# Performance work log

Hardware: AMD Instinct MI355X
Metric: run time of the kernel (lower is better)

Reference implementation:

```python
import jax, jax.numpy as jnp
import numpy as np

C_IN, C_OUT, KH, KW = 64, 128, 3, 3
STRIDE, PAD, DIL = 1, 1, 1
EPS = 1e-5


def setup_inputs() -> dict:
    key = jax.random.key(0)
    ks = jax.random.split(key, 7)
    B, H, W = 8, 112, 112
    x = jax.random.normal(ks[0], (B, C_IN, H, W), dtype=jnp.float32)
    # offset conv: produces 2*KH*KW offset channels; small init keeps offsets sane
    w_off = jax.random.normal(ks[1], (2 * KH * KW, C_IN, KH, KW), dtype=jnp.float32) * 0.01
    b_off = jax.random.normal(ks[2], (2 * KH * KW,), dtype=jnp.float32) * 0.01
    # deformable conv weight/bias
    fan_in = C_IN * KH * KW
    w_dcn = jax.random.normal(ks[3], (C_OUT, C_IN, KH, KW), dtype=jnp.float32) / np.sqrt(fan_in)
    b_dcn = jax.random.normal(ks[4], (C_OUT,), dtype=jnp.float32) * 0.01
    gamma = jnp.ones((C_OUT,), dtype=jnp.float32)
    beta = jnp.zeros((C_OUT,), dtype=jnp.float32)
    return {"x": x, "w_off": w_off, "b_off": b_off, "w_dcn": w_dcn,
            "b_dcn": b_dcn, "gamma": gamma, "beta": beta}


def _conv2d(x, w, b):
    y = jax.lax.conv_general_dilated(
        x, w, window_strides=(STRIDE, STRIDE),
        padding=((PAD, PAD), (PAD, PAD)),
        rhs_dilation=(DIL, DIL),
        dimension_numbers=("NCHW", "OIHW", "NCHW"))
    return y + b[None, :, None, None]


def _deform_conv(x, offset, w, b):
    # x: [B,C,H,W]; offset: [B, 2*KH*KW, Ho, Wo] with (dy, dx) pairs per tap
    B, C, H, W = x.shape
    KK = KH * KW
    Ho, Wo = offset.shape[2], offset.shape[3]
    off = offset.reshape(B, KK, 2, Ho, Wo)
    ky = (jnp.arange(KK) // KW).astype(jnp.float32)  # kernel row per tap
    kx = (jnp.arange(KK) % KW).astype(jnp.float32)
    base_y = (jnp.arange(Ho) * STRIDE - PAD).astype(jnp.float32)
    base_x = (jnp.arange(Wo) * STRIDE - PAD).astype(jnp.float32)
    # sampling positions [B, KK, Ho, Wo]
    py = off[:, :, 0] + base_y[None, None, :, None] + (ky * DIL)[None, :, None, None]
    px = off[:, :, 1] + base_x[None, None, None, :] + (kx * DIL)[None, :, None, None]

    y0 = jnp.floor(py)
    x0 = jnp.floor(px)
    wy1 = py - y0  # weight for y0+1
    wx1 = px - x0
    y0i = y0.astype(jnp.int32)
    x0i = x0.astype(jnp.int32)

    x_flat = x.reshape(B, C, H * W)

    def gather_corner(yi, xi, wgt):
        # yi, xi, wgt: [B, KK, Ho, Wo]
        valid = (yi >= 0) & (yi < H) & (xi >= 0) & (xi < W)
        idx = jnp.clip(yi, 0, H - 1) * W + jnp.clip(xi, 0, W - 1)
        idx = idx.reshape(B, -1)  # [B, KK*Ho*Wo]
        vals = jnp.take_along_axis(x_flat, idx[:, None, :], axis=2)  # [B, C, N]
        coef = (wgt * valid.astype(wgt.dtype)).reshape(B, 1, -1)
        return vals * coef

    samp = (gather_corner(y0i,     x0i,     (1 - wy1) * (1 - wx1))
            + gather_corner(y0i,     x0i + 1, (1 - wy1) * wx1)
            + gather_corner(y0i + 1, x0i,     wy1 * (1 - wx1))
            + gather_corner(y0i + 1, x0i + 1, wy1 * wx1))
    samp = samp.reshape(B, C, KK, Ho, Wo)
    out = jnp.einsum("bckhw,ock->bohw", samp, w.reshape(w.shape[0], C, KK))
    return out + b[None, :, None, None]


def reference(x, w_off, b_off, w_dcn, b_dcn, gamma, beta):
    offset = _conv2d(x, w_off, b_off)
    y = _deform_conv(x, offset, w_dcn, b_dcn)
    # BatchNorm2d (training mode: biased batch stats) + ReLU
    mean = jnp.mean(y, axis=(0, 2, 3))
    var = jnp.var(y, axis=(0, 2, 3))
    yhat = (y - mean[None, :, None, None]) * jax.lax.rsqrt(var + EPS)[None, :, None, None]
    y = gamma[None, :, None, None] * yhat + beta[None, :, None, None]
    return jax.nn.relu(y)
```

## Files before the change

kernel.cpp:

```cpp
#include <hip/hip_runtime.h>

#define H    112
#define W    112
#define HW   12544
#define CIN  64
#define COUT 128
#define BATCH 8
#define KK   9
#define OFFC 18
#define EPS  1e-5f
#define TP   32
#define KDIM 576
#define KHALF 288
#define KPAD2 296
#define NB   3136
#define YST  40
#define SSTRIDE 16

typedef unsigned short ushort;
typedef unsigned int uint;
typedef __attribute__((ext_vector_type(8))) short short8;
typedef __attribute__((ext_vector_type(4))) float floatx4;
typedef __attribute__((ext_vector_type(2))) float f32x2;

__device__ __forceinline__ ushort f2bf(float f) {
  uint u = __float_as_uint(f);
  u = (u + 0x7FFFu + ((u >> 16) & 1u)) >> 16;
  return (ushort)u;
}

__device__ __forceinline__ uint pack_bf2(float f0, float f1) {
  uint u0 = __float_as_uint(f0) + 0x8000u;
  uint u1 = __float_as_uint(f1) + 0x8000u;
  return __builtin_amdgcn_perm(u1, u0, 0x07060302u);
}

__device__ __forceinline__ f32x2 up2(uint u) {
  f32x2 r;
  r.x = __uint_as_float(u << 16);
  r.y = __uint_as_float(u & 0xFFFF0000u);
  return r;
}

__device__ __forceinline__ int tile196(int bx) {
  int xcd = bx & 7, q = bx >> 3;
  return (xcd < 4) ? xcd * 25 + q : 100 + (xcd - 4) * 24 + q;
}

__global__ __launch_bounds__(256) void k_prep(
    const float* __restrict__ x, const float* __restrict__ w_off,
    const float* __restrict__ w_dcn, ushort* __restrict__ xTb,
    ushort* __restrict__ w_offT, ushort* __restrict__ w_mf,
    float* __restrict__ stats) {
  if (blockIdx.y < BATCH) {
    __shared__ float tile[64][65];
    int b = blockIdx.y;
    int p0 = tile196(blockIdx.x) * 64;
    int tid = threadIdx.x;
    int j = tid & 63, cb = tid >> 6;
#pragma unroll
    for (int i = 0; i < 16; ++i) {
      int ci = cb * 16 + i;
      tile[ci][j] = x[((size_t)(b * CIN + ci)) * HW + p0 + j];
    }
    __syncthreads();
    int px = tid >> 2, ciq = tid & 3;
#pragma unroll
    for (int g = 0; g < 4; ++g) {
      int ci = ciq * 16 + g * 4;
      uint lo = pack_bf2(tile[ci + 0][px], tile[ci + 1][px]);
      uint hi = pack_bf2(tile[ci + 2][px], tile[ci + 3][px]);
      *(uint2*)&xTb[((size_t)b * HW + p0 + px) * 64 + ci] = make_uint2(lo, hi);
    }
  } else {
    int tid = threadIdx.x;
    if (blockIdx.x == 0) {
#pragma unroll
      for (int i = tid; i < 256 * SSTRIDE; i += 256) stats[i] = 0.f;
    }
    const int TOT = 32 * KDIM + COUT * KDIM;
    for (int i = blockIdx.x * 256 + tid; i < TOT; i += 196 * 256) {
      if (i < 32 * KDIM) {
        int oc = i / KDIM, k = i - oc * KDIM;
        int kk = k >> 6, ci = k & 63;
        float v = (oc < OFFC) ? w_off[(oc * CIN + ci) * KK + kk] : 0.f;
        w_offT[i] = f2bf(v);
      } else {
        int jj = i - 32 * KDIM;
        int co = jj / KDIM, k = jj - co * KDIM;
        int h2 = k / KHALF, r = k - h2 * KHALF;
        int kk = r >> 5, cil = r & 31;
        int ci = h2 * 32 + cil;
        w_mf[jj] = f2bf(w_dcn[(co * CIN + ci) * KK + kk]);
      }
    }
  }
}

__global__ __launch_bounds__(256) void k_offset_conv(
    const ushort* __restrict__ xTb, const ushort* __restrict__ w_offT,
    const float* __restrict__ bias, float* __restrict__ out) {
  int b = blockIdx.y;
  int wave = threadIdx.x >> 6, lane = threadIdx.x & 63;
  int row16 = lane & 15, quad = lane >> 4;
  int p = tile196(blockIdx.x) * 64 + wave * 16 + row16;
  int ho = p / W, wo = p - ho * W;
  const ushort* xb = xTb + (size_t)b * HW * 64;

  short8 Bf[18];
#pragma unroll
  for (int ks = 0; ks < 18; ++ks) {
    int kk = ks >> 1;
    int ci0 = (ks & 1) * 32 + quad * 8;
    int kh = kk / 3, kw = kk - kh * 3;
    int yy = ho + kh - 1, xx = wo + kw - 1;
    bool valid = (yy >= 0) & (yy < H) & (xx >= 0) & (xx < W);
    short8 v = {0, 0, 0, 0, 0, 0, 0, 0};
    if (valid) v = *(const short8*)(xb + ((size_t)(yy * W + xx) << 6) + ci0);
    Bf[ks] = v;
  }
  floatx4 acc0 = {0.f, 0.f, 0.f, 0.f}, acc1 = acc0;
  const ushort* wa0 = w_offT + row16 * KDIM + quad * 8;
  const ushort* wa1 = w_offT + (16 + row16) * KDIM + quad * 8;
#pragma unroll
  for (int ks = 0; ks < 18; ++ks) {
    short8 A0 = *(const short8*)(wa0 + ks * 32);
    short8 A1 = *(const short8*)(wa1 + ks * 32);
    acc0 = __builtin_amdgcn_mfma_f32_16x16x32_bf16(A0, Bf[ks], acc0, 0, 0, 0);
    acc1 = __builtin_amdgcn_mfma_f32_16x16x32_bf16(A1, Bf[ks], acc1, 0, 0, 0);
  }
  float* ob = out + (size_t)b * OFFC * HW;
#pragma unroll
  for (int reg = 0; reg < 4; ++reg) {
    int oc = quad * 4 + reg;
    ob[(size_t)oc * HW + p] = acc0[reg] + bias[oc];
    int oc1 = 16 + oc;
    if (oc1 < OFFC) ob[(size_t)oc1 * HW + p] = acc1[reg] + bias[oc1];
  }
}

__global__ __launch_bounds__(256, 4) void k_deform(
    const ushort* __restrict__ xTb, const float* __restrict__ off,
    const ushort* __restrict__ w_mf, ushort* __restrict__ y,
    float* __restrict__ psT) {
  __shared__ float4  s_w[KK][TP];
  __shared__ ushort4 s_ip[KK][TP];
  __shared__ __align__(16) char smem_raw[TP * KPAD2 * 2];
  ushort (*samp)[KPAD2] = (ushort(*)[KPAD2])smem_raw;

  int b = blockIdx.y;
  int tile = ((blockIdx.x & 7) * 49) + (blockIdx.x >> 3);
  int p0 = tile * TP;
  int bid = blockIdx.y * gridDim.x + tile;
  int tid = threadIdx.x;
  const ushort* xb = xTb + (size_t)b * HW * 64;

  for (int it = tid; it < KK * TP; it += 256) {
    int kk = it >> 5;
    int px = it & 31;
    int p = p0 + px;
    int ho = p / W, wo = p - ho * W;
    float dy = off[((size_t)b * OFFC + 2 * kk) * HW + p];
    float dx = off[((size_t)b * OFFC + 2 * kk + 1) * HW + p];
    float py = dy + (float)(ho - 1 + kk / 3);
    float pxx = dx + (float)(wo - 1 + kk % 3);
    float y0f = floorf(py), x0f = floorf(pxx);
    float wy1 = py - y0f, wx1 = pxx - x0f;
    int y0 = (int)y0f, x0 = (int)x0f;
    int y1 = y0 + 1, x1 = x0 + 1;
    float vy0 = (y0 >= 0 && y0 < H) ? 1.f : 0.f;
    float vy1 = (y1 >= 0 && y1 < H) ? 1.f : 0.f;
    float vx0 = (x0 >= 0 && x0 < W) ? 1.f : 0.f;
    float vx1 = (x1 >= 0 && x1 < W) ? 1.f : 0.f;
    int cy0 = min(max(y0, 0), H - 1), cy1 = min(max(y1, 0), H - 1);
    int cx0 = min(max(x0, 0), W - 1), cx1 = min(max(x1, 0), W - 1);
    s_w[kk][px] = make_float4((1.f - wy1) * (1.f - wx1) * vy0 * vx0,
                              (1.f - wy1) * wx1 * vy0 * vx1,
                              wy1 * (1.f - wx1) * vy1 * vx0,
                              wy1 * wx1 * vy1 * vx1);
    s_ip[kk][px] = make_ushort4((ushort)(cy0 * W + cx0), (ushort)(cy0 * W + cx1),
                                (ushort)(cy1 * W + cx0), (ushort)(cy1 * W + cx1));
  }
  __syncthreads();

  int wave = tid >> 6, lane = tid & 63;
  int row16 = lane & 15, quad = lane >> 4;
  int koff = quad * 8;
  int co_base = wave * 32;
  const ushort* wa0 = w_mf + (size_t)(co_base + row16) * KDIM + koff;
  const ushort* wa1 = w_mf + (size_t)(co_base + 16 + row16) * KDIM + koff;

  floatx4 acc00 = {0.f, 0.f, 0.f, 0.f}, acc01 = acc00, acc10 = acc00, acc11 = acc00;

  for (int h = 0; h < 2; ++h) {
    uint4 c0v[5], c1v[5], c2v[5], c3v[5];
#pragma unroll
    for (int r = 0; r < 5; ++r) {
      int it = tid + r * 256;
      if (it < KK * TP * 4) {
        int kk = it >> 7;
        int px = (it >> 2) & 31;
        int cig = it & 3;
        int cio = h * 32 + cig * 8;
        ushort4 ip = s_ip[kk][px];
        c0v[r] = *(const uint4*)(xb + (((int)ip.x) << 6) + cio);
        c1v[r] = *(const uint4*)(xb + (((int)ip.y) << 6) + cio);
        c2v[r] = *(const uint4*)(xb + (((int)ip.z) << 6) + cio);
        c3v[r] = *(const uint4*)(xb + (((int)ip.w) << 6) + cio);
      }
    }
#pragma unroll
    for (int r = 0; r < 5; ++r) {
      int it = tid + r * 256;
      if (it < KK * TP * 4) {
        int kk = it >> 7;
        int px = (it >> 2) & 31;
        int cig = it & 3;
        int cil0 = cig * 8;
        float4 wv = s_w[kk][px];
        uint4 c0 = c0v[r], c1 = c1v[r], c2 = c2v[r], c3 = c3v[r];
        f32x2 r0 = up2(c0.x) * wv.x + up2(c1.x) * wv.y + up2(c2.x) * wv.z + up2(c3.x) * wv.w;
        f32x2 r1 = up2(c0.y) * wv.x + up2(c1.y) * wv.y + up2(c2.y) * wv.z + up2(c3.y) * wv.w;
        f32x2 r2 = up2(c0.z) * wv.x + up2(c1.z) * wv.y + up2(c2.z) * wv.z + up2(c3.z) * wv.w;
        f32x2 r3 = up2(c0.w) * wv.x + up2(c1.w) * wv.y + up2(c2.w) * wv.z + up2(c3.w) * wv.w;
        *(uint4*)&samp[px][kk * 32 + cil0] =
            make_uint4(pack_bf2(r0.x, r0.y), pack_bf2(r1.x, r1.y),
                       pack_bf2(r2.x, r2.y), pack_bf2(r3.x, r3.y));
      }
    }
    __syncthreads();

    const ushort* sb0 = &samp[row16][koff];
    const ushort* sb1 = &samp[16 + row16][koff];
    const ushort* a0 = wa0 + h * KHALF;
    const ushort* a1 = wa1 + h * KHALF;
#pragma unroll
    for (int ks = 0; ks < 9; ++ks) {
      short8 A0 = *(const short8*)(a0 + ks * 32);
      short8 A1 = *(const short8*)(a1 + ks * 32);
      short8 B0 = *(const short8*)(sb0 + ks * 32);
      short8 B1 = *(const short8*)(sb1 + ks * 32);
      acc00 = __builtin_amdgcn_mfma_f32_16x16x32_bf16(A0, B0, acc00, 0, 0, 0);
      acc01 = __builtin_amdgcn_mfma_f32_16x16x32_bf16(A0, B1, acc01, 0, 0, 0);
      acc10 = __builtin_amdgcn_mfma_f32_16x16x32_bf16(A1, B0, acc10, 0, 0, 0);
      acc11 = __builtin_amdgcn_mfma_f32_16x16x32_bf16(A1, B1, acc11, 0, 0, 0);
    }
    __syncthreads();
  }

  ushort (*yst)[YST] = (ushort(*)[YST])smem_raw;
#pragma unroll
  for (int reg = 0; reg < 4; ++reg) {
    int r0 = quad * 4 + reg;
    yst[co_base + r0][row16]            = f2bf(acc00[reg]);
    yst[co_base + r0][16 + row16]       = f2bf(acc01[reg]);
    yst[co_base + 16 + r0][row16]       = f2bf(acc10[reg]);
    yst[co_base + 16 + r0][16 + row16]  = f2bf(acc11[reg]);
  }
#pragma unroll
  for (int reg = 0; reg < 4; ++reg) {
    float s0 = acc00[reg] + acc01[reg];
    float q0 = acc00[reg] * acc00[reg] + acc01[reg] * acc01[reg];
    float s1 = acc10[reg] + acc11[reg];
    float q1 = acc10[reg] * acc10[reg] + acc11[reg] * acc11[reg];
#pragma unroll
    for (int m = 1; m < 16; m <<= 1) {
      s0 += __shfl_xor(s0, m, 64);
      q0 += __shfl_xor(q0, m, 64);
      s1 += __shfl_xor(s1, m, 64);
      q1 += __shfl_xor(q1, m, 64);
    }
    if (row16 == 0) {
      int c0 = co_base + quad * 4 + reg;
      float* pb = psT + (size_t)bid * 256;
      pb[c0] = s0;
      pb[COUT + c0] = q0;
      pb[c0 + 16] = s1;
      pb[COUT + c0 + 16] = q1;
    }
  }
  __syncthreads();
  {
    int co = tid >> 1, hf = tid & 1;
    const ushort* src = &yst[co][hf * 16];
    uint4 v0 = *(const uint4*)src;
    uint4 v1 = *(const uint4*)(src + 8);
    ushort* dst = y + (size_t)b * COUT * HW + (size_t)co * HW + p0 + hf * 16;
    *(uint4*)dst = v0;
    *(uint4*)(dst + 8) = v1;
  }
}

__global__ __launch_bounds__(256) void k_reduce(const float* __restrict__ psT,
                                                float* __restrict__ stats) {
  int c = threadIdx.x;
  float s = 0.f;
  for (int r = blockIdx.x; r < NB; r += gridDim.x)
    s += psT[(size_t)r * 256 + c];
  atomicAdd(&stats[(size_t)c * SSTRIDE], s);
}

__global__ __launch_bounds__(256) void k_norm(const ushort* __restrict__ y,
                                              const float* __restrict__ stats,
                                              const float* __restrict__ gamma,
                                              const float* __restrict__ beta,
                                              float* __restrict__ out) {
  int i4 = blockIdx.x * 256 + threadIdx.x;
  const int total4 = BATCH * COUT * HW / 4;
  if (i4 >= total4) return;
  size_t i = (size_t)i4 * 4;
  int c = (int)((i / HW) & (COUT - 1));
  const float N = (float)(BATCH * HW);
  float m = stats[(size_t)c * SSTRIDE] / N;
  float var = stats[(size_t)(COUT + c) * SSTRIDE] / N - m * m;
  float r = rsqrtf(var + EPS);
  float g = gamma[c], bt = beta[c];
  uint2 u = *(const uint2*)&y[i];
  float4 v = make_float4(__uint_as_float(u.x << 16), __uint_as_float(u.x & 0xFFFF0000u),
                         __uint_as_float(u.y << 16), __uint_as_float(u.y & 0xFFFF0000u));
  v.x = fmaxf(0.f, (v.x - m) * r * g + bt);
  v.y = fmaxf(0.f, (v.y - m) * r * g + bt);
  v.z = fmaxf(0.f, (v.z - m) * r * g + bt);
  v.w = fmaxf(0.f, (v.w - m) * r * g + bt);
  *(float4*)&out[i] = v;
}

extern "C" void kernel_launch(void* const* d_in, const int* in_sizes, int n_in,
                              void* d_out, int out_size, void* d_ws, size_t ws_size,
                              hipStream_t stream) {
  const float* x     = (const float*)d_in[0];
  const float* w_off = (const float*)d_in[1];
  const float* b_off = (const float*)d_in[2];
  const float* w_dcn = (const float*)d_in[3];
  const float* gamma = (const float*)d_in[5];
  const float* beta  = (const float*)d_in[6];
  float* out = (float*)d_out;

  float* ws = (float*)d_ws;
  float*  off_buf = ws;
  float*  psT     = off_buf + 1806336;
  float*  stats   = psT + 802816;
  ushort* xTb     = (ushort*)(stats + 256 * SSTRIDE);
  ushort* w_mf    = xTb + (size_t)BATCH * HW * 64;
  ushort* w_offT  = w_mf + COUT * KDIM;
  ushort* y_bf    = w_offT + 32 * KDIM;

  k_prep<<<dim3(196, 9), 256, 0, stream>>>(x, w_off, w_dcn, xTb, w_offT, w_mf, stats);
  k_offset_conv<<<dim3(HW / 64, BATCH), 256, 0, stream>>>(xTb, w_offT, b_off, off_buf);
  k_deform<<<dim3(HW / TP, BATCH), 256, 0, stream>>>(xTb, off_buf, w_mf, y_bf, psT);
  k_reduce<<<32, 256, 0, stream>>>(psT, stats);
  k_norm<<<BATCH * COUT * HW / 4 / 256, 256, 0, stream>>>(y_bf, stats, gamma, beta, out);
}
```

Baseline: 249.4 us.

## Fuse offset conv into prep kernel reading fp32 input directly

```diff
diff --git a/kernel.cpp b/kernel.cpp
--- a/kernel.cpp
+++ b/kernel.cpp
@@ -35,6 +35,13 @@
   return __builtin_amdgcn_perm(u1, u0, 0x07060302u);
 }
 
+__device__ __forceinline__ short8 pack8(const float* v) {
+  union { short8 s; uint4 u; } cv;
+  cv.u = make_uint4(pack_bf2(v[0], v[1]), pack_bf2(v[2], v[3]),
+                    pack_bf2(v[4], v[5]), pack_bf2(v[6], v[7]));
+  return cv.s;
+}
+
 __device__ __forceinline__ f32x2 up2(uint u) {
   f32x2 r;
   r.x = __uint_as_float(u << 16);
@@ -49,14 +56,14 @@
 
 __global__ __launch_bounds__(256) void k_prep(
     const float* __restrict__ x, const float* __restrict__ w_off,
-    const float* __restrict__ w_dcn, ushort* __restrict__ xTb,
-    ushort* __restrict__ w_offT, ushort* __restrict__ w_mf,
-    float* __restrict__ stats) {
+    const float* __restrict__ b_off, const float* __restrict__ w_dcn,
+    ushort* __restrict__ xTb, ushort* __restrict__ w_mf,
+    float* __restrict__ stats, float* __restrict__ off_buf) {
+  int tid = threadIdx.x;
   if (blockIdx.y < BATCH) {
     __shared__ float tile[64][65];
     int b = blockIdx.y;
     int p0 = tile196(blockIdx.x) * 64;
-    int tid = threadIdx.x;
     int j = tid & 63, cb = tid >> 6;
 #pragma unroll
     for (int i = 0; i < 16; ++i) {
@@ -72,74 +79,73 @@
       uint hi = pack_bf2(tile[ci + 2][px], tile[ci + 3][px]);
       *(uint2*)&xTb[((size_t)b * HW + p0 + px) * 64 + ci] = make_uint2(lo, hi);
     }
+  } else if (blockIdx.y < 2 * BATCH) {
+    int b = blockIdx.y - BATCH;
+    int wave = tid >> 6, lane = tid & 63;
+    int row16 = lane & 15, quad = lane >> 4;
+    int p = tile196(blockIdx.x) * 64 + wave * 16 + row16;
+    int ho = p / W, wo = p - ho * W;
+    const float* xb = x + (size_t)b * CIN * HW;
+
+    short8 Bf[18];
+#pragma unroll
+    for (int ks = 0; ks < 18; ++ks) {
+      int kk = ks >> 1;
+      int ci0 = (ks & 1) * 32 + quad * 8;
+      int kh = kk / 3, kw = kk - kh * 3;
+      int yy = ho + kh - 1, xx = wo + kw - 1;
+      bool valid = (yy >= 0) & (yy < H) & (xx >= 0) & (xx < W);
+      float v[8];
+#pragma unroll
+      for (int j = 0; j < 8; ++j)
+        v[j] = valid ? xb[(size_t)(ci0 + j) * HW + yy * W + xx] : 0.f;
+      Bf[ks] = pack8(v);
+    }
+    floatx4 acc0 = {0.f, 0.f, 0.f, 0.f}, acc1 = acc0;
+#pragma unroll
+    for (int ks = 0; ks < 18; ++ks) {
+      int kk = ks >> 1;
+      int ci0 = (ks & 1) * 32 + quad * 8;
+      const float* wr = w_off + kk;
+      float a[8];
+#pragma unroll
+      for (int j = 0; j < 8; ++j)
+        a[j] = wr[(row16 * CIN + ci0 + j) * KK];
+      short8 A0 = pack8(a);
+      short8 A1 = {0, 0, 0, 0, 0, 0, 0, 0};
+      if (row16 < OFFC - 16) {
+#pragma unroll
+        for (int j = 0; j < 8; ++j)
+          a[j] = wr[((16 + row16) * CIN + ci0 + j) * KK];
+        A1 = pack8(a);
+      }
+      acc0 = __builtin_amdgcn_mfma_f32_16x16x32_bf16(A0, Bf[ks], acc0, 0, 0, 0);
+      acc1 = __builtin_amdgcn_mfma_f32_16x16x32_bf16(A1, Bf[ks], acc1, 0, 0, 0);
+    }
+    float* ob = off_buf + (size_t)b * OFFC * HW;
+#pragma unroll
+    for (int reg = 0; reg < 4; ++reg) {
+      int oc = quad * 4 + reg;
+      ob[(size_t)oc * HW + p] = acc0[reg] + b_off[oc];
+      int oc1 = 16 + oc;
+      if (oc1 < OFFC) ob[(size_t)oc1 * HW + p] = acc1[reg] + b_off[oc1];
+    }
   } else {
-    int tid = threadIdx.x;
     if (blockIdx.x == 0) {
 #pragma unroll
       for (int i = tid; i < 256 * SSTRIDE; i += 256) stats[i] = 0.f;
     }
-    const int TOT = 32 * KDIM + COUT * KDIM;
-    for (int i = blockIdx.x * 256 + tid; i < TOT; i += 196 * 256) {
-      if (i < 32 * KDIM) {
-        int oc = i / KDIM, k = i - oc * KDIM;
-        int kk = k >> 6, ci = k & 63;
-        float v = (oc < OFFC) ? w_off[(oc * CIN + ci) * KK + kk] : 0.f;
-        w_offT[i] = f2bf(v);
-      } else {
-        int jj = i - 32 * KDIM;
-        int co = jj / KDIM, k = jj - co * KDIM;
-        int h2 = k / KHALF, r = k - h2 * KHALF;
-        int kk = r >> 5, cil = r & 31;
-        int ci = h2 * 32 + cil;
-        w_mf[jj] = f2bf(w_dcn[(co * CIN + ci) * KK + kk]);
-      }
-    }
-  }
-}
-
-__global__ __launch_bounds__(256) void k_offset_conv(
-    const ushort* __restrict__ xTb, const ushort* __restrict__ w_offT,
-    const float* __restrict__ bias, float* __restrict__ out) {
-  int b = blockIdx.y;
-  int wave = threadIdx.x >> 6, lane = threadIdx.x & 63;
-  int row16 = lane & 15, quad = lane >> 4;
-  int p = tile196(blockIdx.x) * 64 + wave * 16 + row16;
-  int ho = p / W, wo = p - ho * W;
-  const ushort* xb = xTb + (size_t)b * HW * 64;
-
-  short8 Bf[18];
-#pragma unroll
-  for (int ks = 0; ks < 18; ++ks) {
-    int kk = ks >> 1;
-    int ci0 = (ks & 1) * 32 + quad * 8;
-    int kh = kk / 3, kw = kk - kh * 3;
-    int yy = ho + kh - 1, xx = wo + kw - 1;
-    bool valid = (yy >= 0) & (yy < H) & (xx >= 0) & (xx < W);
-    short8 v = {0, 0, 0, 0, 0, 0, 0, 0};
-    if (valid) v = *(const short8*)(xb + ((size_t)(yy * W + xx) << 6) + ci0);
-    Bf[ks] = v;
-  }
-  floatx4 acc0 = {0.f, 0.f, 0.f, 0.f}, acc1 = acc0;
-  const ushort* wa0 = w_offT + row16 * KDIM + quad * 8;
-  const ushort* wa1 = w_offT + (16 + row16) * KDIM + quad * 8;
-#pragma unroll
-  for (int ks = 0; ks < 18; ++ks) {
-    short8 A0 = *(const short8*)(wa0 + ks * 32);
-    short8 A1 = *(const short8*)(wa1 + ks * 32);
-    acc0 = __builtin_amdgcn_mfma_f32_16x16x32_bf16(A0, Bf[ks], acc0, 0, 0, 0);
-    acc1 = __builtin_amdgcn_mfma_f32_16x16x32_bf16(A1, Bf[ks], acc1, 0, 0, 0);
-  }
-  float* ob = out + (size_t)b * OFFC * HW;
-#pragma unroll
-  for (int reg = 0; reg < 4; ++reg) {
-    int oc = quad * 4 + reg;
-    ob[(size_t)oc * HW + p] = acc0[reg] + bias[oc];
-    int oc1 = 16 + oc;
-    if (oc1 < OFFC) ob[(size_t)oc1 * HW + p] = acc1[reg] + bias[oc1];
-  }
-}
-
-__global__ __launch_bounds__(256, 4) void k_deform(
+    for (int i = blockIdx.x * 256 + tid; i < COUT * KDIM; i += 196 * 256) {
+      int co = i / KDIM, k = i - co * KDIM;
+      int h2 = k / KHALF, r = k - h2 * KHALF;
+      int kk = r >> 5, cil = r & 31;
+      int ci = h2 * 32 + cil;
+      w_mf[i] = f2bf(w_dcn[(co * CIN + ci) * KK + kk]);
+    }
+  }
+}
+
+__global__ __launch_bounds__(256, 6) void k_deform(
     const ushort* __restrict__ xTb, const float* __restrict__ off,
     const ushort* __restrict__ w_mf, ushort* __restrict__ y,
     float* __restrict__ psT) {
@@ -342,11 +348,10 @@
   float*  stats   = psT + 802816;
   ushort* xTb     = (ushort*)(stats + 256 * SSTRIDE);
   ushort* w_mf    = xTb + (size_t)BATCH * HW * 64;
-  ushort* w_offT  = w_mf + COUT * KDIM;
-  ushort* y_bf    = w_offT + 32 * KDIM;
-
-  k_prep<<<dim3(196, 9), 256, 0, stream>>>(x, w_off, w_dcn, xTb, w_offT, w_mf, stats);
-  k_offset_conv<<<dim3(HW / 64, BATCH), 256, 0, stream>>>(xTb, w_offT, b_off, off_buf);
+  ushort* y_bf    = w_mf + COUT * KDIM;
+
+  k_prep<<<dim3(196, 17), 256, 0, stream>>>(x, w_off, b_off, w_dcn,
+                                            xTb, w_mf, stats, off_buf);
   k_deform<<<dim3(HW / TP, BATCH), 256, 0, stream>>>(xTb, off_buf, w_mf, y_bf, psT);
   k_reduce<<<32, 256, 0, stream>>>(psT, stats);
   k_norm<<<BATCH * COUT * HW / 4 / 256, 256, 0, stream>>>(y_bf, stats, gamma, beta, out);
```

New measurement: 487.7 us. 95.6% more time.
